# Kernel tuning notes

Hardware: AMD Instinct MI355X
Metric: run time of the kernel (lower is better)

Reference implementation:

```python
import jax, jax.numpy as jnp
import numpy as np
from jax import lax

DT_REF = 1.0
EPS = 1e-5


def layer_norm(x, g, b):
    m = jnp.mean(x, axis=-1, keepdims=True)
    v = jnp.mean(jnp.square(x - m), axis=-1, keepdims=True)
    return (x - m) * lax.rsqrt(v + EPS) * g + b


def pscan(A, X):
    # linear recurrence y_t = a_t*y_{t-1} + x_t along axis=1 (time)
    def comb(c1, c2):
        a1, x1 = c1
        a2, x2 = c2
        return a1 * a2, a2 * x1 + x2
    return lax.associative_scan(comb, (A, X), axis=1)[1]


def _forward(x_re, x_im, h_re, h_im, dt, flux_re, flux_im,
             ns_g, ns_b, conv_w, conv_b, E_re, E_im, F_re, F_im,
             mix_w, mix_b, nu, theta, src_w, src_b, gate_w, gate_b,
             lam_a, lam_b, nt_g, nt_b, r_w, r_b, e_w1, e_b1, e_w2, e_b2):
    B, T, D, H, W = x_re.shape
    x = lax.complex(x_re, x_im)                       # [B,T,D,H,W] complex

    # ---- spatial process: LN -> Clifford(3x3) conv -> complex residual ----
    xf = x.reshape(B * T, D, H, W)
    xr = jnp.concatenate([xf.real, xf.imag], axis=1)  # [BT,2D,H,W]
    xn = layer_norm(xr.transpose(0, 2, 3, 1), ns_g, ns_b).transpose(0, 3, 1, 2)
    xs = lax.conv_general_dilated(xn, conv_w, (1, 1), 'SAME',
                                  dimension_numbers=('NCHW', 'OIHW', 'NCHW'))
    xs = xs + conv_b[None, :, None, None]
    x = (xf + lax.complex(xs[:, :D], xs[:, D:])).reshape(B, T, D, H, W)

    # ---- eigenbasis encode ----
    Ec = lax.complex(E_re, E_im)                      # [D,D] complex basis
    xp = x.transpose(0, 1, 3, 4, 2)                   # [B,T,H,W,D]
    x_eigen = jnp.einsum('bthwd,de->bthwe', xp, Ec)
    x_mean = jnp.mean(x_eigen, axis=(2, 3))           # [B,T,D]

    # ---- flux tracker scan ----
    decay = jnp.exp(lax.complex(-jax.nn.softplus(nu), theta))  # [D]
    fcat = jnp.concatenate([x_mean.real, x_mean.imag], axis=-1) @ mix_w + mix_b
    x_mixed = lax.complex(fcat[..., :D], fcat[..., D:])        # [B,T,D]
    A_flux = jnp.broadcast_to(decay, (B, T, D))
    flux_seq = pscan(A_flux, x_mixed)                          # [B,T,D]
    decay_cum = jnp.cumprod(A_flux, axis=1)
    flux_seq = flux_seq + lax.complex(flux_re, flux_im)[:, None, :] * decay_cum

    ocat = jnp.concatenate([flux_seq.real, flux_seq.imag], axis=-1)  # [B,T,2D]
    s = ocat @ src_w + src_b
    source = lax.complex(s[..., :D], s[..., D:])                     # [B,T,D]
    gate = jax.nn.sigmoid(ocat @ gate_w + gate_b)                    # [B,T,D] real
    g = gate[:, :, None, None, :]
    forcing = x_eigen * g + source[:, :, None, None, :] * (1.0 - g)  # [B,T,H,W,D]

    # ---- transition operators (ZOH) ----
    dt_exp = jnp.broadcast_to(dt[None, :], (B, T))
    lam = lax.complex(-jax.nn.softplus(lam_a), lam_b)                # [D]
    op_decay = jnp.exp(lam[None, None, :] * (DT_REF * dt_exp)[:, :, None])  # [B,T,D]
    op_forcing = (op_decay - 1.0) / lam[None, None, :]

    u_t = forcing * op_forcing[:, :, None, None, :]
    h_prev = lax.complex(h_re, h_im).reshape(B, H, W, D)
    u_t = u_t.at[:, 0].add(h_prev * op_decay[:, 0][:, None, None, :])

    # ---- per-pixel/per-channel state scan over time ----
    A_state = jnp.broadcast_to(op_decay[:, :, None, None, :], u_t.shape)
    u_out = pscan(A_state, u_t)                       # [B,T,H,W,D]

    # ---- decode + temporal LN + MoE FFN ----
    Fc = lax.complex(F_re, F_im)
    x_dec = jnp.einsum('bthwd,de->bthwe', u_out, Fc)  # [B,T,H,W,D]
    of = x_dec.transpose(0, 1, 4, 2, 3).reshape(B * T, D, H, W)
    oc = jnp.concatenate([of.real, of.imag], axis=1).transpose(0, 2, 3, 1)  # [BT,H,W,2D]
    on = layer_norm(oc, nt_g, nt_b)
    xc = lax.complex(on[..., :D], on[..., D:])        # [BT,H,W,D]

    probs = jax.nn.softmax(on @ r_w + r_b, axis=-1)   # [BT,H,W,E]
    hid = jax.nn.gelu(jnp.einsum('nhwc,ecm->nhwem', on, e_w1) + e_b1)
    eo = jnp.einsum('nhwem,emc->nhwec', hid, e_w2) + e_b2
    moe = jnp.einsum('nhwec,nhwe->nhwc', eo, probs)   # [BT,H,W,2D]
    delta = lax.complex(moe[..., :D], moe[..., D:])

    x_outc = (xc + delta).transpose(0, 3, 1, 2).reshape(B, T, D, H, W)
    z = x + x_outc
    return jnp.concatenate([z.real, z.imag], axis=2)  # [B,T,2D,H,W] real


def setup_inputs() -> dict:
    B, T, D, H, W = 2, 16, 64, 64, 64
    C = 2 * D            # real channel width
    E, M = 4, 2 * C      # num_experts, ffn hidden = expand*2D, expand=2
    key = jax.random.key(0)
    ks = jax.random.split(key, 24)
    r = lambda k, shp, s=0.05: jax.random.normal(k, shp, jnp.float32) * s
    return dict(
        x_re=r(ks[0], (B, T, D, H, W), 0.5), x_im=r(ks[1], (B, T, D, H, W), 0.5),
        h_re=r(ks[2], (B * H * W, 1, D), 0.1), h_im=r(ks[3], (B * H * W, 1, D), 0.1),
        dt=jax.random.uniform(ks[4], (T,), jnp.float32, 0.5, 1.5),
        flux_re=r(ks[5], (B, D), 0.1), flux_im=r(ks[6], (B, D), 0.1),
        ns_g=jnp.ones((C,), jnp.float32), ns_b=jnp.zeros((C,), jnp.float32),
        conv_w=r(ks[7], (C, C, 3, 3)), conv_b=jnp.zeros((C,), jnp.float32),
        E_re=r(ks[8], (D, D), 0.1), E_im=r(ks[9], (D, D), 0.1),
        F_re=r(ks[10], (D, D), 0.1), F_im=r(ks[11], (D, D), 0.1),
        mix_w=r(ks[12], (C, C)), mix_b=jnp.zeros((C,), jnp.float32),
        nu=r(ks[13], (D,), 0.5) + 1.0, theta=r(ks[14], (D,), 0.5),
        src_w=r(ks[15], (C, C)), src_b=jnp.zeros((C,), jnp.float32),
        gate_w=r(ks[16], (C, D)), gate_b=jnp.zeros((D,), jnp.float32),
        lam_a=r(ks[17], (D,), 0.5) + 1.0, lam_b=r(ks[18], (D,), 0.5),
        nt_g=jnp.ones((C,), jnp.float32), nt_b=jnp.zeros((C,), jnp.float32),
        r_w=r(ks[19], (C, E)), r_b=jnp.zeros((E,), jnp.float32),
        e_w1=r(ks[20], (E, C, M)), e_b1=jnp.zeros((E, M), jnp.float32),
        e_w2=r(ks[21], (E, M, C)), e_b2=jnp.zeros((E, C), jnp.float32))


def reference(x_re, x_im, h_re, h_im, dt, flux_re, flux_im,
              ns_g, ns_b, conv_w, conv_b, E_re, E_im, F_re, F_im,
              mix_w, mix_b, nu, theta, src_w, src_b, gate_w, gate_b,
              lam_a, lam_b, nt_g, nt_b, r_w, r_b, e_w1, e_b1, e_w2, e_b2):
    return _forward(x_re, x_im, h_re, h_im, dt, flux_re, flux_im,
                    ns_g, ns_b, conv_w, conv_b, E_re, E_im, F_re, F_im,
                    mix_w, mix_b, nu, theta, src_w, src_b, gate_w, gate_b,
                    lam_a, lam_b, nt_g, nt_b, r_w, r_b, e_w1, e_b1, e_w2, e_b2)
```

## Files before the change

kernel.cpp:

```cpp
#include <hip/hip_runtime.h>


#define DEV static __device__ __forceinline__

typedef __attribute__((ext_vector_type(8))) short bf16x8;
typedef __attribute__((ext_vector_type(4))) float f32x4;
typedef __attribute__((ext_vector_type(16))) float f32x16;
typedef __attribute__((ext_vector_type(4))) unsigned int u32x4;

namespace {
constexpr int TN = 32;

DEV float sp_f(float x) { return x > 20.f ? x : log1pf(expf(x)); }
DEV unsigned short f2bf(float f) {
  unsigned int u = __float_as_uint(f);
  unsigned int r = (u + 0x7FFFu + ((u >> 16) & 1u)) >> 16;
  return (unsigned short)r;
}
DEV float bf2f(unsigned short s) { return __uint_as_float(((unsigned int)s) << 16); }
DEV unsigned int cvtpk(float lo, float hi) {
  unsigned int u;
  asm("v_cvt_pk_bf16_f32 %0, %1, %2" : "=v"(u) : "v"(lo), "v"(hi));
  return u;
}
DEV void split2(float a, float b, unsigned int& hi, unsigned int& lo) {
  unsigned short ha = f2bf(a), hb = f2bf(b);
  hi = (unsigned int)ha | ((unsigned int)hb << 16);
  float la = a - bf2f(ha), lb = b - bf2f(hb);
  lo = (unsigned int)f2bf(la) | ((unsigned int)f2bf(lb) << 16);
}
DEV float exp2_asm(float x) {
  float r;
  asm("v_exp_f32 %0, %1" : "=v"(r) : "v"(x));
  return r;
}
DEV float gelu_f(float x) {
  float e = exp2_asm(-2.4554863f * x);
  return x * __builtin_amdgcn_rcpf(1.f + e);
}
}

__global__ void k_repc(const float* __restrict__ cw, unsigned short* __restrict__ wcv) {
  int i = blockIdx.x * 256 + threadIdx.x;
  if (i >= 9 * 4 * 8 * 64 * 8) return;
  int j = i & 7, l = (i >> 3) & 63, ct = (i >> 9) & 7, cb = (i >> 12) & 3, k = i >> 14;
  int co = ct * 16 + (l & 15);
  int ci = cb * 32 + (l >> 4) * 8 + j;
  wcv[i] = f2bf(cw[((size_t)co * 128 + ci) * 9 + k]);
}

__global__ void k_repw(const float* __restrict__ w1, const float* __restrict__ w2,
                       const float* __restrict__ rw,
                       unsigned short* __restrict__ w1tp, unsigned short* __restrict__ w2p32,
                       unsigned short* __restrict__ rwp) {
  int i = blockIdx.x * 256 + threadIdx.x;
  if (i >= 262144 + 2048) return;
  if (i >= 262144) {
    int idx = i - 262144;
    int j = idx & 7, l = (idx >> 3) & 63, kt = idx >> 9;
    int col = l & 15;
    rwp[idx] = col < 4 ? f2bf(rw[(kt * 32 + (l >> 4) * 8 + j) * 4 + col]) : (unsigned short)0;
    return;
  }
  int half = i >> 17;
  int idx = i & 131071;
  int j = idx & 7, l = (idx >> 3) & 63;
  if (half == 0) {
    int kt = (idx >> 9) & 7, mtG = (idx >> 12) & 7, e = idx >> 15;
    int c = kt * 16 + (l >> 5) * 8 + j, m = mtG * 32 + (l & 31);
    w1tp[idx] = f2bf(w1[((size_t)e * 128 + c) * 256 + m]);
  } else {
    int ct = (idx >> 9) & 3, ktG = (idx >> 11) & 15, e = idx >> 15;
    int m = ktG * 16 + (l >> 5) * 8 + j, c = ct * 32 + (l & 31);
    w2p32[idx] = f2bf(w2[((size_t)e * 256 + m) * 128 + c]);
  }
}

__global__ void k_repEF(const float* __restrict__ Ere, const float* __restrict__ Eim,
                        const float* __restrict__ Fre, const float* __restrict__ Fim,
                        unsigned short* __restrict__ efb) {
  int i = blockIdx.x * 256 + threadIdx.x;
  if (i >= 32768) return;
  int sel = i >> 14;
  int f = i & 16383;
  float val;
  if (f < 8192) {
    int j = f & 7, l = (f >> 3) & 63, kt = (f >> 9) & 1, es = (f >> 10) & 1;
    int v = (f >> 11) & 1, eh = f >> 12;
    int d = kt * 32 + (l >> 4) * 8 + j;
    int e = eh * 32 + es * 16 + (l & 15);
    val = (v ? Eim : Ere)[d * 64 + e];
  } else {
    int g = f - 8192;
    int j = g & 7, l = (g >> 3) & 63, ds = (g >> 9) & 3;
    int v = (g >> 11) & 1, eh = g >> 12;
    int e = eh * 32 + (l >> 4) * 8 + j;
    int d = ds * 16 + (l & 15);
    val = (v ? Fim : Fre)[e * 64 + d];
  }
  unsigned short hv = f2bf(val);
  efb[i] = sel ? f2bf(val - bf2f(hv)) : hv;
}

__global__ __launch_bounds__(256) void k_ln_in(
    const float* __restrict__ xre, const float* __restrict__ xim,
    const float* __restrict__ gg, const float* __restrict__ bb,
    unsigned short* __restrict__ xnb, unsigned short* __restrict__ xfb) {
  int n = blockIdx.x >> 6, h = blockIdx.x & 63;
  __shared__ float xl[64][129];
  __shared__ float ps[4][64], ps2[4][64];
  __shared__ float mu[64], rs[64];
  int tid = threadIdx.x;
  int w = tid & 63, q = tid >> 6;
  size_t base = ((size_t)n * 4096 + h) * 64 + w;
  for (int d = q; d < 64; d += 4) {
    size_t o = base + (size_t)d * 4096;
    xl[w][d] = xre[o];
    xl[w][64 + d] = xim[o];
  }
  __syncthreads();
  float s = 0.f, s2 = 0.f;
  for (int c = q * 32; c < q * 32 + 32; ++c) { float v = xl[w][c]; s += v; s2 += v * v; }
  ps[q][w] = s; ps2[q][w] = s2;
  __syncthreads();
  if (tid < 64) {
    float a = 0.f, b2 = 0.f;
#pragma unroll
    for (int i = 0; i < 4; ++i) { a += ps[i][tid]; b2 += ps2[i][tid]; }
    float m = a * (1.f / 128.f);
    mu[tid] = m;
    rs[tid] = rsqrtf(b2 * (1.f / 128.f) - m * m + 1e-5f);
  }
  __syncthreads();
  size_t obase = ((size_t)n * 4096 + (size_t)h * 64) * 128;
  for (int idx = tid; idx < 64 * 64; idx += 256) {
    int q2 = idx >> 6, c2 = (idx & 63) * 2;
    float r0 = xl[q2][c2], r1 = xl[q2][c2 + 1];
    float v0 = (r0 - mu[q2]) * rs[q2] * gg[c2] + bb[c2];
    float v1 = (r1 - mu[q2]) * rs[q2] * gg[c2 + 1] + bb[c2 + 1];
    *(unsigned int*)&xnb[obase + (size_t)q2 * 128 + c2] = cvtpk(v0, v1);
    *(unsigned int*)&xfb[obase + (size_t)q2 * 128 + c2] = cvtpk(r0, r1);
  }
}

__global__ __launch_bounds__(256) void k_conv(
    const unsigned short* __restrict__ xnb, const unsigned short* __restrict__ wcv,
    const float* __restrict__ cbias, const unsigned short* __restrict__ xfb,
    unsigned short* __restrict__ XSf, unsigned short* __restrict__ XSl) {
  int n = blockIdx.x >> 6, h = blockIdx.x & 63;
  __shared__ __align__(16) short in_t[3 * 66 * 128];
  __shared__ float tr[64][66];
  int tid = threadIdx.x;
  int l = tid & 63;
  int w = __builtin_amdgcn_readfirstlane(tid >> 6);

  for (int it = 0; it < 13; ++it) {
    int ch = tid + it * 256;
    if (ch < 3168) {
      int ri = ch >> 4, cb16 = ch & 15;
      int rr = ri >= 132 ? 2 : (ri >= 66 ? 1 : 0);
      int wp = ri - rr * 66 - 1;
      int hh = h + rr - 1;
      uint4 v = make_uint4(0, 0, 0, 0);
      if ((unsigned)hh < 64u && (unsigned)wp < 64u)
        v = *(const uint4*)(xnb + ((size_t)(n * 4096 + hh * 64 + wp) << 7) + cb16 * 8);
      int off = (ri * 256 + cb16 * 16) ^ ((ri & 7) << 4);
      *(uint4*)((char*)in_t + off) = v;
    }
  }
  __syncthreads();

  f32x4 acc[4][2];
#pragma unroll
  for (int pt = 0; pt < 4; ++pt) { acc[pt][0] = {0,0,0,0}; acc[pt][1] = {0,0,0,0}; }

#pragma unroll
  for (int kh = 0; kh < 3; ++kh) {
#pragma unroll
    for (int kw = 0; kw < 3; ++kw) {
      int k = kh * 3 + kw;
#pragma unroll
      for (int cb = 0; cb < 4; ++cb) {
        const unsigned short* wb = wcv + ((((size_t)(k * 4 + cb) * 8) + 2 * w) * 64 + l) * 8;
        bf16x8 b0 = *(const bf16x8*)wb;
        bf16x8 b1 = *(const bf16x8*)(wb + 64 * 8);
#pragma unroll
        for (int pt = 0; pt < 4; ++pt) {
          int ri = kh * 66 + pt * 16 + (l & 15) + kw;
          int off = (ri * 256 + cb * 64 + (l >> 4) * 16) ^ ((ri & 7) << 4);
          bf16x8 a = *(const bf16x8*)((const char*)in_t + off);
          acc[pt][0] = __builtin_amdgcn_mfma_f32_16x16x32_bf16(a, b0, acc[pt][0], 0, 0, 0);
          acc[pt][1] = __builtin_amdgcn_mfma_f32_16x16x32_bf16(a, b1, acc[pt][1], 0, 0, 0);
        }
      }
    }
  }

  for (int pass = 0; pass < 2; ++pass) {
    __syncthreads();
    if ((w >> 1) == pass) {
      int ctl = w & 1;
#pragma unroll
      for (int ct = 0; ct < 2; ++ct) {
        int col = ctl * 32 + ct * 16 + (l & 15);
        float bias = cbias[pass * 64 + col];
#pragma unroll
        for (int pt = 0; pt < 4; ++pt) {
          int pxb = pt * 16 + (l >> 4) * 4;
          size_t xfo = ((size_t)(n * 4096 + h * 64 + pxb)) * 128 + pass * 64 + col;
#pragma unroll
          for (int r = 0; r < 4; ++r)
            tr[col][pxb + r] = acc[pt][ct][r] + bias + bf2f(xfb[xfo + (size_t)r * 128]);
        }
      }
    }
    __syncthreads();
#pragma unroll
    for (int q = 0; q < 2; ++q) {
      int it = tid + q * 256;
      int ptl = it >> 7, kt = (it >> 6) & 1, lf = it & 63;
      int dbase = kt * 32 + (lf >> 4) * 8;
      int px = ptl * 16 + (lf & 15);
      unsigned int hw[4], lw[4];
#pragma unroll
      for (int u = 0; u < 4; ++u)
        split2(tr[dbase + 2 * u][px], tr[dbase + 2 * u + 1][px], hw[u], lw[u]);
      size_t base = ((((size_t)n * 256 + h * 4 + ptl) * 2 + pass) * 2 + kt) * 512 + lf * 8;
      *(uint4*)(XSf + base) = make_uint4(hw[0], hw[1], hw[2], hw[3]);
      *(uint4*)(XSl + base) = make_uint4(lw[0], lw[1], lw[2], lw[3]);
    }
    __syncthreads();
  }
}

__global__ __launch_bounds__(256) void k_xmean(const unsigned short* __restrict__ XSf,
                                               const unsigned short* __restrict__ XSl,
                                               float2* __restrict__ Xm) {
  int nd = blockIdx.x;
  int n = nd >> 6, d = nd & 63;
  int kt = d >> 5, hs = (d >> 3) & 3, j = d & 7;
  int tid = threadIdx.x;
  float sr = 0.f, si = 0.f;
  for (int p = tid; p < 4096; p += 256) {
    int ptg = p >> 4, c = p & 15;
    size_t b0 = ((((size_t)n * 256 + ptg) * 2 + 0) * 2 + kt) * 512 + (hs * 16 + c) * 8 + j;
    size_t b1 = ((((size_t)n * 256 + ptg) * 2 + 1) * 2 + kt) * 512 + (hs * 16 + c) * 8 + j;
    sr += bf2f(XSf[b0]) + bf2f(XSl[b0]);
    si += bf2f(XSf[b1]) + bf2f(XSl[b1]);
  }
  __shared__ float r1[256], r2[256];
  r1[tid] = sr; r2[tid] = si;
  __syncthreads();
  for (int s = 128; s > 0; s >>= 1) {
    if (tid < s) { r1[tid] += r1[tid + s]; r2[tid] += r2[tid + s]; }
    __syncthreads();
  }
  if (tid == 0) Xm[nd] = make_float2(r1[0] * (1.f / 4096.f), r2[0] * (1.f / 4096.f));
}

__global__ void k_chainA(const float2* __restrict__ Xm, const float* __restrict__ Ere,
                         const float* __restrict__ Eim, const float* __restrict__ mixw,
                         const float* __restrict__ mixb, float2* __restrict__ xmix) {
  int n = blockIdx.x;
  int tid = threadIdx.x;
  __shared__ float2 xm[64];
  __shared__ float cat[128];
  __shared__ float fc[128];
  if (tid < 64) xm[tid] = Xm[n * 64 + tid];
  __syncthreads();
  if (tid < 64) {
    float ar = 0.f, ai = 0.f;
    for (int d = 0; d < 64; ++d) {
      float2 x = xm[d];
      float er = Ere[d * 64 + tid], ei = Eim[d * 64 + tid];
      ar += x.x * er - x.y * ei;
      ai += x.x * ei + x.y * er;
    }
    cat[tid] = ar; cat[64 + tid] = ai;
  }
  __syncthreads();
  {
    float f = mixb[tid];
    for (int i = 0; i < 128; ++i) f += cat[i] * mixw[i * 128 + tid];
    fc[tid] = f;
  }
  __syncthreads();
  if (tid < 64) xmix[n * 64 + tid] = make_float2(fc[tid], fc[64 + tid]);
}

__global__ void k_chainB(const float2* __restrict__ xmix, const float* __restrict__ nu,
                         const float* __restrict__ th, const float* __restrict__ fre,
                         const float* __restrict__ fim, float2* __restrict__ fs) {
  int tid = threadIdx.x;
  int b = tid >> 6, d = tid & 63;
  float r = expf(-sp_f(nu[d]));
  float dr = r * cosf(th[d]), di = r * sinf(th[d]);
  float yr = 0.f, yi = 0.f, cr = 1.f, ci = 0.f;
  float fr = fre[b * 64 + d], fi = fim[b * 64 + d];
  for (int t = 0; t < 16; ++t) {
    int n = b * 16 + t;
    float ncr = cr * dr - ci * di, nci = cr * di + ci * dr;
    cr = ncr; ci = nci;
    float2 xm = xmix[n * 64 + d];
    float nyr = dr * yr - di * yi + xm.x;
    float nyi = dr * yi + di * yr + xm.y;
    yr = nyr; yi = nyi;
    fs[n * 64 + d] = make_float2(yr + fr * cr - fi * ci, yi + fr * ci + fi * cr);
  }
}

__global__ void k_chainC(const float2* __restrict__ fs, const float* __restrict__ srcw,
                         const float* __restrict__ srcb, const float* __restrict__ gw,
                         const float* __restrict__ gbv, const float* __restrict__ la,
                         const float* __restrict__ lbv, const float* __restrict__ dt,
                         float* __restrict__ abo) {
  int n = blockIdx.x;
  int t = n & 15;
  int tid = threadIdx.x;
  __shared__ float oc[128];
  __shared__ float sl[128];
  if (tid < 64) { float2 v = fs[n * 64 + tid]; oc[tid] = v.x; oc[64 + tid] = v.y; }
  __syncthreads();
  {
    float s = srcb[tid];
    for (int i = 0; i < 128; ++i) s += oc[i] * srcw[i * 128 + tid];
    sl[tid] = s;
  }
  __syncthreads();
  if (tid < 64) {
    float gv = gbv[tid];
    for (int i = 0; i < 128; ++i) gv += oc[i] * gw[i * 64 + tid];
    float g = 1.f / (1.f + expf(-gv));
    float lr = -sp_f(la[tid]), li = lbv[tid];
    float dtv = dt[t];
    float er = expf(lr * dtv);
    float odr = er * cosf(li * dtv), odi = er * sinf(li * dtv);
    float inv = 1.f / (lr * lr + li * li);
    float nx = odr - 1.f, ny = odi;
    float ofr = (nx * lr + ny * li) * inv, ofi = (ny * lr - nx * li) * inv;
    float s1r = sl[tid] * (1.f - g), s1i = sl[64 + tid] * (1.f - g);
    float* ap = abo + ((size_t)n * 64 + tid) * 8;
    ap[0] = g * ofr;
    ap[1] = g * ofi;
    ap[2] = s1r * ofr - s1i * ofi;
    ap[3] = s1r * ofi + s1i * ofr;
    ap[4] = odr;
    ap[5] = odi;
    ap[6] = 0.f; ap[7] = 0.f;
  }
}

__global__ __launch_bounds__(128) void k_state(
    const unsigned short* __restrict__ XSf, const unsigned short* __restrict__ XSl,
    const unsigned short* __restrict__ efb,
    const float* __restrict__ abo, const float* __restrict__ hre,
    const float* __restrict__ him, const float* __restrict__ ntg,
    const float* __restrict__ ntb, unsigned short* __restrict__ onb) {
  int bq = blockIdx.x;
  int b = bq >> 8, pt = bq & 255;
  int p0 = pt * 16;
  int tid = threadIdx.x;
  int l = tid & 63;
  int eh = __builtin_amdgcn_readfirstlane(tid >> 6);
  int c = l & 15, h4 = l >> 4;

  __shared__ float xpart[2 * 64 * 17];
  __shared__ float ntgl[128], ntbl[128];
  ntgl[tid] = ntg[tid]; ntbl[tid] = ntb[tid];

  const unsigned short* Ehi = efb;
  const unsigned short* Fhi = efb + 8192;
  const unsigned short* Elo = efb + 16384;
  const unsigned short* Flo = efb + 24576;

  bf16x8 erh[2][2], eihh[2][2], erl[2][2], eil[2][2];
#pragma unroll
  for (int es = 0; es < 2; ++es)
#pragma unroll
    for (int kt = 0; kt < 2; ++kt) {
      size_t o = (size_t)(eh * 4096 + es * 1024 + kt * 512 + l * 8);
      erh[es][kt] = *(const bf16x8*)(Ehi + o);
      eihh[es][kt] = *(const bf16x8*)(Ehi + o + 2048);
      erl[es][kt] = *(const bf16x8*)(Elo + o);
      eil[es][kt] = *(const bf16x8*)(Elo + o + 2048);
    }
  bf16x8 frh[4], fih[4], frl[4], fil[4];
#pragma unroll
  for (int ds = 0; ds < 4; ++ds) {
    size_t o = (size_t)(eh * 4096 + ds * 512 + l * 8);
    frh[ds] = *(const bf16x8*)(Fhi + o);
    fih[ds] = *(const bf16x8*)(Fhi + o + 2048);
    frl[ds] = *(const bf16x8*)(Flo + o);
    fil[ds] = *(const bf16x8*)(Flo + o + 2048);
  }

  float yre[2][4], yim[2][4];
#pragma unroll
  for (int es = 0; es < 2; ++es)
#pragma unroll
    for (int r = 0; r < 4; ++r) { yre[es][r] = 0.f; yim[es][r] = 0.f; }

  __syncthreads();

  const f32x4 Z = {0.f, 0.f, 0.f, 0.f};
  for (int t = 0; t < 16; ++t) {
    int n = b * 16 + t;
    bf16x8 xh0[2], xh1[2], xq0[2], xq1[2];
#pragma unroll
    for (int kt = 0; kt < 2; ++kt) {
      size_t b0 = ((((size_t)n * 256 + pt) * 2 + 0) * 2 + kt) * 512 + l * 8;
      size_t b1 = ((((size_t)n * 256 + pt) * 2 + 1) * 2 + kt) * 512 + l * 8;
      xh0[kt] = *(const bf16x8*)(XSf + b0);
      xh1[kt] = *(const bf16x8*)(XSf + b1);
      xq0[kt] = *(const bf16x8*)(XSl + b0);
      xq1[kt] = *(const bf16x8*)(XSl + b1);
    }
#pragma unroll
    for (int es = 0; es < 2; ++es) {
      f32x4 a1 = Z, a2 = Z, a3 = Z, a4 = Z;
#pragma unroll
      for (int kt = 0; kt < 2; ++kt) {
        a1 = __builtin_amdgcn_mfma_f32_16x16x32_bf16(erh[es][kt], xh0[kt], a1, 0, 0, 0);
        a1 = __builtin_amdgcn_mfma_f32_16x16x32_bf16(erh[es][kt], xq0[kt], a1, 0, 0, 0);
        a1 = __builtin_amdgcn_mfma_f32_16x16x32_bf16(erl[es][kt], xh0[kt], a1, 0, 0, 0);
        a2 = __builtin_amdgcn_mfma_f32_16x16x32_bf16(eihh[es][kt], xh1[kt], a2, 0, 0, 0);
        a2 = __builtin_amdgcn_mfma_f32_16x16x32_bf16(eihh[es][kt], xq1[kt], a2, 0, 0, 0);
        a2 = __builtin_amdgcn_mfma_f32_16x16x32_bf16(eil[es][kt], xh1[kt], a2, 0, 0, 0);
        a3 = __builtin_amdgcn_mfma_f32_16x16x32_bf16(eihh[es][kt], xh0[kt], a3, 0, 0, 0);
        a3 = __builtin_amdgcn_mfma_f32_16x16x32_bf16(eihh[es][kt], xq0[kt], a3, 0, 0, 0);
        a3 = __builtin_amdgcn_mfma_f32_16x16x32_bf16(eil[es][kt], xh0[kt], a3, 0, 0, 0);
        a4 = __builtin_amdgcn_mfma_f32_16x16x32_bf16(erh[es][kt], xh1[kt], a4, 0, 0, 0);
        a4 = __builtin_amdgcn_mfma_f32_16x16x32_bf16(erh[es][kt], xq1[kt], a4, 0, 0, 0);
        a4 = __builtin_amdgcn_mfma_f32_16x16x32_bf16(erl[es][kt], xh1[kt], a4, 0, 0, 0);
      }
#pragma unroll
      for (int r = 0; r < 4; ++r) {
        int e = eh * 32 + es * 16 + 4 * h4 + r;
        const float* ap = abo + ((size_t)n * 64 + e) * 8;
        float4 cv = *(const float4*)ap;
        float2 ov = *(const float2*)(ap + 4);
        float xr_ = a1[r] - a2[r], xi_ = a3[r] + a4[r];
        float ur = xr_ * cv.x - xi_ * cv.y + cv.z;
        float ui = xr_ * cv.y + xi_ * cv.x + cv.w;
        if (t == 0) {
          size_t ho = ((size_t)(b * 4096 + p0 + c)) * 64 + e;
          float hr = hre[ho], hi = him[ho];
          ur += hr * ov.x - hi * ov.y;
          ui += hr * ov.y + hi * ov.x;
        }
        float nyr = ov.x * yre[es][r] - ov.y * yim[es][r] + ur;
        float nyi = ov.x * yim[es][r] + ov.y * yre[es][r] + ui;
        yre[es][r] = nyr; yim[es][r] = nyi;
      }
    }
    unsigned int hr_[2][2], lr_[2][2], hi_[2][2], li_[2][2];
#pragma unroll
    for (int es = 0; es < 2; ++es) {
      split2(yre[es][0], yre[es][1], hr_[es][0], lr_[es][0]);
      split2(yre[es][2], yre[es][3], hr_[es][1], lr_[es][1]);
      split2(yim[es][0], yim[es][1], hi_[es][0], li_[es][0]);
      split2(yim[es][2], yim[es][3], hi_[es][1], li_[es][1]);
    }
    int base_src = c + 16 * (2 * (h4 & 1));
    int hsel = h4 >> 1;
    u32x4 urh, uih, url, uil;
#pragma unroll
    for (int jj = 0; jj < 4; ++jj) {
      int src = base_src + 16 * (jj >> 1);
      unsigned int t0, t1;
      t0 = (unsigned int)__shfl((int)hr_[0][jj & 1], src);
      t1 = (unsigned int)__shfl((int)hr_[1][jj & 1], src);
      urh[jj] = hsel ? t1 : t0;
      t0 = (unsigned int)__shfl((int)hi_[0][jj & 1], src);
      t1 = (unsigned int)__shfl((int)hi_[1][jj & 1], src);
      uih[jj] = hsel ? t1 : t0;
      t0 = (unsigned int)__shfl((int)lr_[0][jj & 1], src);
      t1 = (unsigned int)__shfl((int)lr_[1][jj & 1], src);
      url[jj] = hsel ? t1 : t0;
      t0 = (unsigned int)__shfl((int)li_[0][jj & 1], src);
      t1 = (unsigned int)__shfl((int)li_[1][jj & 1], src);
      uil[jj] = hsel ? t1 : t0;
    }
    bf16x8 ybrh = __builtin_bit_cast(bf16x8, urh);
    bf16x8 ybih = __builtin_bit_cast(bf16x8, uih);
    bf16x8 ybrl = __builtin_bit_cast(bf16x8, url);
    bf16x8 ybil = __builtin_bit_cast(bf16x8, uil);
    float v[2][4][4];
#pragma unroll
    for (int ds = 0; ds < 4; ++ds) {
      f32x4 d1 = Z, d2 = Z, d3 = Z, d4 = Z;
      d1 = __builtin_amdgcn_mfma_f32_16x16x32_bf16(frh[ds], ybrh, d1, 0, 0, 0);
      d1 = __builtin_amdgcn_mfma_f32_16x16x32_bf16(frh[ds], ybrl, d1, 0, 0, 0);
      d1 = __builtin_amdgcn_mfma_f32_16x16x32_bf16(frl[ds], ybrh, d1, 0, 0, 0);
      d2 = __builtin_amdgcn_mfma_f32_16x16x32_bf16(fih[ds], ybih, d2, 0, 0, 0);
      d2 = __builtin_amdgcn_mfma_f32_16x16x32_bf16(fih[ds], ybil, d2, 0, 0, 0);
      d2 = __builtin_amdgcn_mfma_f32_16x16x32_bf16(fil[ds], ybih, d2, 0, 0, 0);
      d3 = __builtin_amdgcn_mfma_f32_16x16x32_bf16(fih[ds], ybrh, d3, 0, 0, 0);
      d3 = __builtin_amdgcn_mfma_f32_16x16x32_bf16(fih[ds], ybrl, d3, 0, 0, 0);
      d3 = __builtin_amdgcn_mfma_f32_16x16x32_bf16(fil[ds], ybrh, d3, 0, 0, 0);
      d4 = __builtin_amdgcn_mfma_f32_16x16x32_bf16(frh[ds], ybih, d4, 0, 0, 0);
      d4 = __builtin_amdgcn_mfma_f32_16x16x32_bf16(frh[ds], ybil, d4, 0, 0, 0);
      d4 = __builtin_amdgcn_mfma_f32_16x16x32_bf16(frl[ds], ybih, d4, 0, 0, 0);
#pragma unroll
      for (int r = 0; r < 4; ++r) {
        v[0][ds][r] = d1[r] - d2[r];
        v[1][ds][r] = d3[r] + d4[r];
      }
    }
    bool own = (eh == (t & 1));
    if (!own) {
#pragma unroll
      for (int p = 0; p < 2; ++p)
#pragma unroll
        for (int ds = 0; ds < 4; ++ds)
#pragma unroll
          for (int r = 0; r < 4; ++r)
            xpart[(p * 64 + ds * 16 + 4 * h4 + r) * 17 + c] = v[p][ds][r];
    }
    __syncthreads();
    if (own) {
      float s = 0.f, s2 = 0.f;
#pragma unroll
      for (int p = 0; p < 2; ++p)
#pragma unroll
        for (int ds = 0; ds < 4; ++ds)
#pragma unroll
          for (int r = 0; r < 4; ++r) {
            float q2 = v[p][ds][r] + xpart[(p * 64 + ds * 16 + 4 * h4 + r) * 17 + c];
            v[p][ds][r] = q2;
            s += q2; s2 += q2 * q2;
          }
      s += __shfl_xor(s, 16); s += __shfl_xor(s, 32);
      s2 += __shfl_xor(s2, 16); s2 += __shfl_xor(s2, 32);
      float mu = s * (1.f / 128.f);
      float rsv = rsqrtf(s2 * (1.f / 128.f) - mu * mu + 1e-5f);
      size_t ob = ((size_t)(n * 4096 + p0 + c)) * 128;
#pragma unroll
      for (int p = 0; p < 2; ++p)
#pragma unroll
        for (int ds = 0; ds < 4; ++ds) {
          int ch = p * 64 + ds * 16 + 4 * h4;
          float l0 = (v[p][ds][0] - mu) * rsv * ntgl[ch + 0] + ntbl[ch + 0];
          float l1 = (v[p][ds][1] - mu) * rsv * ntgl[ch + 1] + ntbl[ch + 1];
          float l2 = (v[p][ds][2] - mu) * rsv * ntgl[ch + 2] + ntbl[ch + 2];
          float l3 = (v[p][ds][3] - mu) * rsv * ntgl[ch + 3] + ntbl[ch + 3];
          *(unsigned int*)&onb[ob + ch] = cvtpk(l0, l1);
          *(unsigned int*)&onb[ob + ch + 2] = cvtpk(l2, l3);
        }
    }
    __syncthreads();
  }
}

__global__ __launch_bounds__(256) void k_moe2(
    const unsigned short* __restrict__ onb, const unsigned short* __restrict__ w1tp,
    const unsigned short* __restrict__ w2p32, const unsigned short* __restrict__ rwp,
    const float* __restrict__ rb, const float* __restrict__ b1, const float* __restrict__ b2,
    const unsigned short* __restrict__ XSf, const unsigned short* __restrict__ XSl,
    float* __restrict__ out) {
  int n = blockIdx.x >> 6, ptile = blockIdx.x & 63;
  int p0 = ptile * 64;
  __shared__ __align__(16) short At[64 * 128];
  __shared__ __align__(16) float buf[4160];
  __shared__ float pr[64][4];
  int tid = threadIdx.x;
  int l = tid & 63;
  int w = __builtin_amdgcn_readfirstlane(tid >> 6);
  int h = l >> 5, s = l & 31;
  float* b1l = buf;
  float* b2l = buf + 1024;

  for (int i = tid; i < 1024; i += 256) b1l[i] = b1[i];
  for (int i = tid; i < 512; i += 256) b2l[i] = b2[i];

  {
    const char* gsrc = (const char*)onb + ((size_t)n * 4096 + p0) * 256;
#pragma unroll
    for (int it = 0; it < 4; ++it) {
      int ch = tid + it * 256;
      int row = ch >> 4, cb = (ch & 15) * 16;
      float4 v = *(const float4*)(gsrc + (size_t)row * 256 + cb);
      int off = (row * 256 + cb) ^ ((row & 7) << 4);
      *(float4*)((char*)At + off) = v;
    }
  }
  __syncthreads();

  {
    f32x4 acc = {0.f, 0.f, 0.f, 0.f};
#pragma unroll
    for (int kt = 0; kt < 4; ++kt) {
      int row = w * 16 + (l & 15);
      int off = (row * 256 + kt * 64 + (l >> 4) * 16) ^ ((row & 7) << 4);
      bf16x8 aa = *(const bf16x8*)((const char*)At + off);
      bf16x8 bb = *(const bf16x8*)(rwp + ((size_t)kt * 64 + l) * 8);
      acc = __builtin_amdgcn_mfma_f32_16x16x32_bf16(aa, bb, acc, 0, 0, 0);
    }
    int e = l & 15;
    float rbv = e < 4 ? rb[e] : 0.f;
#pragma unroll
    for (int r = 0; r < 4; ++r) {
      float lg = acc[r] + rbv;
      float m = fmaxf(lg, __shfl_xor(lg, 1));
      m = fmaxf(m, __shfl_xor(m, 2));
      float ex = __expf(lg - m);
      float sm = ex + __shfl_xor(ex, 1);
      sm += __shfl_xor(sm, 2);
      float p = ex * __builtin_amdgcn_rcpf(sm);
      if (e < 4) pr[w * 16 + (l >> 4) * 4 + r][e] = p;
    }
  }
  __syncthreads();

  int pw = w & 1, mh = w >> 1;
  int rowb = pw * 32 + s;
  int swz = (rowb & 7) << 4;

  float macc[4][16];
#pragma unroll
  for (int ct = 0; ct < 4; ++ct)
#pragma unroll
    for (int r = 0; r < 16; ++r) macc[ct][r] = 0.f;

  const f32x16 Z16 = {0.f, 0.f, 0.f, 0.f, 0.f, 0.f, 0.f, 0.f,
                      0.f, 0.f, 0.f, 0.f, 0.f, 0.f, 0.f, 0.f};

  for (int e = 0; e < 4; ++e) {
    u32x4 af[8];
#pragma unroll
    for (int mt = 0; mt < 4; ++mt) {
      f32x16 acc = Z16;
#pragma unroll
      for (int kt = 0; kt < 8; ++kt) {
        bf16x8 a = *(const bf16x8*)(
            w1tp + ((((size_t)e * 8 + (mh * 4 + mt)) * 8 + kt) * 64 + l) * 8);
        int off = (rowb * 256 + kt * 32 + h * 16) ^ swz;
        bf16x8 b = *(const bf16x8*)((const char*)At + off);
        acc = __builtin_amdgcn_mfma_f32_32x32x16_bf16(a, b, acc, 0, 0, 0);
      }
      unsigned int hpk[8];
#pragma unroll
      for (int i2 = 0; i2 < 8; ++i2) {
        int r0 = 2 * i2;
        int m0 = mh * 128 + mt * 32 + (r0 & 3) + 8 * (r0 >> 2) + 4 * h;
        float2 bv = *(const float2*)&b1l[e * 256 + m0];
        hpk[i2] = cvtpk(gelu_f(acc[r0] + bv.x), gelu_f(acc[r0 + 1] + bv.y));
      }
#pragma unroll
      for (int hf = 0; hf < 2; ++hf) {
        unsigned int pA = hpk[4 * hf + 0], pB = hpk[4 * hf + 1];
        unsigned int pC = hpk[4 * hf + 2], pD = hpk[4 * hf + 3];
        unsigned int Z0 = h ? pC : pA, Z1 = h ? pD : pB;
        unsigned int S0 = h ? pA : pC, S1 = h ? pB : pD;
        unsigned int Ss0 = (unsigned int)__shfl_xor((int)S0, 32);
        unsigned int Ss1 = (unsigned int)__shfl_xor((int)S1, 32);
        u32x4 fr2;
        fr2.x = h ? Ss0 : Z0;
        fr2.y = h ? Ss1 : Z1;
        fr2.z = h ? Z0 : Ss0;
        fr2.w = h ? Z1 : Ss1;
        af[mt * 2 + hf] = fr2;
      }
    }
    float prv[16];
#pragma unroll
    for (int r = 0; r < 16; ++r) {
      int px = pw * 32 + (r & 3) + 8 * (r >> 2) + 4 * h;
      prv[r] = pr[px][e];
    }
#pragma unroll
    for (int ct = 0; ct < 4; ++ct) {
      f32x16 acc = Z16;
#pragma unroll
      for (int kt = 0; kt < 8; ++kt) {
        bf16x8 bf = *(const bf16x8*)(
            w2p32 + ((((size_t)e * 16 + (mh * 8 + kt)) * 4 + ct) * 64 + l) * 8);
        bf16x8 a = __builtin_bit_cast(bf16x8, af[kt]);
        acc = __builtin_amdgcn_mfma_f32_32x32x16_bf16(a, bf, acc, 0, 0, 0);
      }
      float b2v = mh ? 0.f : b2l[e * 128 + ct * 32 + s];
#pragma unroll
      for (int r = 0; r < 16; ++r) macc[ct][r] += (acc[r] + b2v) * prv[r];
    }
  }

#pragma unroll
  for (int ph = 0; ph < 2; ++ph) {
    int ct0 = ph * 2;
    __syncthreads();
    if (mh == 1) {
#pragma unroll
      for (int g = 0; g < 8; ++g) {
        int ct = ct0 + (g >> 2), q = (g & 3) * 4;
        float4 v = make_float4(macc[ct][q], macc[ct][q + 1], macc[ct][q + 2], macc[ct][q + 3]);
        *(float4*)&buf[((g * 2 + pw) * 64 + l) * 4] = v;
      }
    }
    __syncthreads();
    if (mh == 0) {
#pragma unroll
      for (int g = 0; g < 8; ++g) {
        float4 v = *(const float4*)&buf[((g * 2 + pw) * 64 + l) * 4];
        int ct = ct0 + (g >> 2), q = (g & 3) * 4;
        macc[ct][q] += v.x; macc[ct][q + 1] += v.y;
        macc[ct][q + 2] += v.z; macc[ct][q + 3] += v.w;
      }
    }
    __syncthreads();
    if (mh == 0) {
#pragma unroll
      for (int cti = 0; cti < 2; ++cti) {
        int ct = ct0 + cti;
        int cc = ct * 32 + s;
        int cl = cc - ph * 64;
#pragma unroll
        for (int r = 0; r < 16; ++r) {
          int px = pw * 32 + (r & 3) + 8 * (r >> 2) + 4 * h;
          int aoff = (px * 256 + cc * 2) ^ ((px & 7) << 4);
          float onv = bf2f(((unsigned short*)At)[aoff >> 1]);
          buf[px * 65 + cl] = macc[ct][r] + onv;
        }
      }
    }
    __syncthreads();
    for (int idx = tid; idx < 64 * 64; idx += 256) {
      int px = idx & 63, cl = idx >> 6;
      int p = p0 + px;
      size_t el = ((((size_t)n * 256 + (p >> 4)) * 2 + ph) * 2 + (cl >> 5)) * 512
                + (((cl >> 3) & 3) * 16 + (p & 15)) * 8 + (cl & 7);
      float resid = bf2f(XSf[el]) + bf2f(XSl[el]);
      out[((size_t)n * 128 + ph * 64 + cl) * 4096 + p0 + px] = resid + buf[px * 65 + cl];
    }
  }
}

extern "C" void kernel_launch(void* const* d_in, const int* in_sizes, int n_in,
                              void* d_out, int out_size, void* d_ws, size_t ws_size,
                              hipStream_t stream) {
  const float* xre = (const float*)d_in[0];
  const float* xim = (const float*)d_in[1];
  const float* hre = (const float*)d_in[2];
  const float* him = (const float*)d_in[3];
  const float* dt = (const float*)d_in[4];
  const float* fre = (const float*)d_in[5];
  const float* fim = (const float*)d_in[6];
  const float* nsg = (const float*)d_in[7];
  const float* nsb = (const float*)d_in[8];
  const float* cw = (const float*)d_in[9];
  const float* cb = (const float*)d_in[10];
  const float* Ere = (const float*)d_in[11];
  const float* Eim = (const float*)d_in[12];
  const float* Fre = (const float*)d_in[13];
  const float* Fim = (const float*)d_in[14];
  const float* mixw = (const float*)d_in[15];
  const float* mixb = (const float*)d_in[16];
  const float* nu = (const float*)d_in[17];
  const float* th = (const float*)d_in[18];
  const float* srcw = (const float*)d_in[19];
  const float* srcb = (const float*)d_in[20];
  const float* gw = (const float*)d_in[21];
  const float* gbv = (const float*)d_in[22];
  const float* la = (const float*)d_in[23];
  const float* lb = (const float*)d_in[24];
  const float* ntg = (const float*)d_in[25];
  const float* ntb = (const float*)d_in[26];
  const float* rw = (const float*)d_in[27];
  const float* rb = (const float*)d_in[28];
  const float* w1 = (const float*)d_in[29];
  const float* b1 = (const float*)d_in[30];
  const float* w2 = (const float*)d_in[31];
  const float* b2 = (const float*)d_in[32];

  unsigned short* XSf = (unsigned short*)d_ws;
  unsigned short* XSl = XSf + 16777216;
  unsigned short* onb16 = XSl + 16777216;
  unsigned short* wcv = onb16 + 16777216;
  unsigned short* w1tp = wcv + 147456;
  unsigned short* w2p32 = w1tp + 131072;
  unsigned short* rwp = w2p32 + 131072;
  unsigned short* efb = rwp + 2048;
  float* smf = (float*)(efb + 32768);
  float* abo = smf;
  float2* Xm = (float2*)(abo + 16384);
  float2* xmix = Xm + TN * 64;
  float2* fsb = xmix + TN * 64;

  float* out = (float*)d_out;
  unsigned short* xnb = (unsigned short*)d_out;
  unsigned short* xfb = xnb + 16777216;

  hipLaunchKernelGGL(k_repc, dim3(576), dim3(256), 0, stream, cw, wcv);
  hipLaunchKernelGGL(k_repw, dim3(1033), dim3(256), 0, stream, w1, w2, rw, w1tp, w2p32, rwp);
  hipLaunchKernelGGL(k_repEF, dim3(128), dim3(256), 0, stream, Ere, Eim, Fre, Fim, efb);
  hipLaunchKernelGGL(k_ln_in, dim3(TN * 64), dim3(256), 0, stream, xre, xim, nsg, nsb, xnb, xfb);
  hipLaunchKernelGGL(k_conv, dim3(TN * 64), dim3(256), 0, stream, xnb, wcv, cb, xfb, XSf, XSl);
  hipLaunchKernelGGL(k_xmean, dim3(TN * 64), dim3(256), 0, stream, XSf, XSl, Xm);
  hipLaunchKernelGGL(k_chainA, dim3(TN), dim3(128), 0, stream, Xm, Ere, Eim, mixw, mixb, xmix);
  hipLaunchKernelGGL(k_chainB, dim3(1), dim3(128), 0, stream, xmix, nu, th, fre, fim, fsb);
  hipLaunchKernelGGL(k_chainC, dim3(TN), dim3(128), 0, stream, fsb, srcw, srcb, gw, gbv, la, lb,
                     dt, abo);
  hipLaunchKernelGGL(k_state, dim3(512), dim3(128), 0, stream, XSf, XSl, efb, abo, hre, him,
                     ntg, ntb, onb16);
  hipLaunchKernelGGL(k_moe2, dim3(TN * 64), dim3(256), 0, stream, onb16, w1tp, w2p32, rwp, rb,
                     b1, b2, XSf, XSl, out);
  (void)in_sizes; (void)n_in; (void)out_size; (void)ws_size;
}
```

Before: 500.0 us.

## Fold MoE gate probability into hidden activations and accumulate experts in MFMA

The router probability now scales the GELU hidden activations (per token row) before the second GEMM, so all experts accumulate directly into one set of MFMA accumulators instead of per-expert temporaries that were scaled and added by hand. The second GEMM is interleaved into the first's loop, so the af fragment array no longer has to stay live. The b2 bias weighted by the probabilities is added once in the epilogue from a new shared array. This cuts VALU multiply-adds and register pressure, at the cost of rounding the probability-scaled activations to bf16.

```diff
diff --git a/kernel.cpp b/kernel.cpp
--- a/kernel.cpp
+++ b/kernel.cpp
@@ -563,15 +563,15 @@
   __shared__ __align__(16) short At[64 * 128];
   __shared__ __align__(16) float buf[4160];
   __shared__ float pr[64][4];
+  __shared__ float b2ls[512];
   int tid = threadIdx.x;
   int l = tid & 63;
   int w = __builtin_amdgcn_readfirstlane(tid >> 6);
   int h = l >> 5, s = l & 31;
   float* b1l = buf;
-  float* b2l = buf + 1024;
 
   for (int i = tid; i < 1024; i += 256) b1l[i] = b1[i];
-  for (int i = tid; i < 512; i += 256) b2l[i] = b2[i];
+  for (int i = tid; i < 512; i += 256) b2ls[i] = b2[i];
 
   {
     const char* gsrc = (const char*)onb + ((size_t)n * 4096 + p0) * 256;
@@ -616,17 +616,14 @@
   int rowb = pw * 32 + s;
   int swz = (rowb & 7) << 4;
 
-  float macc[4][16];
-#pragma unroll
-  for (int ct = 0; ct < 4; ++ct)
-#pragma unroll
-    for (int r = 0; r < 16; ++r) macc[ct][r] = 0.f;
-
   const f32x16 Z16 = {0.f, 0.f, 0.f, 0.f, 0.f, 0.f, 0.f, 0.f,
                       0.f, 0.f, 0.f, 0.f, 0.f, 0.f, 0.f, 0.f};
+  f32x16 macc4[4];
+#pragma unroll
+  for (int ct = 0; ct < 4; ++ct) macc4[ct] = Z16;
 
   for (int e = 0; e < 4; ++e) {
-    u32x4 af[8];
+    float pe = pr[rowb][e];
 #pragma unroll
     for (int mt = 0; mt < 4; ++mt) {
       f32x16 acc = Z16;
@@ -644,7 +641,7 @@
         int r0 = 2 * i2;
         int m0 = mh * 128 + mt * 32 + (r0 & 3) + 8 * (r0 >> 2) + 4 * h;
         float2 bv = *(const float2*)&b1l[e * 256 + m0];
-        hpk[i2] = cvtpk(gelu_f(acc[r0] + bv.x), gelu_f(acc[r0 + 1] + bv.y));
+        hpk[i2] = cvtpk(gelu_f(acc[r0] + bv.x) * pe, gelu_f(acc[r0 + 1] + bv.y) * pe);
       }
 #pragma unroll
       for (int hf = 0; hf < 2; ++hf) {
@@ -659,28 +656,15 @@
         fr2.y = h ? Ss1 : Z1;
         fr2.z = h ? Z0 : Ss0;
         fr2.w = h ? Z1 : Ss1;
-        af[mt * 2 + hf] = fr2;
-      }
-    }
-    float prv[16];
-#pragma unroll
-    for (int r = 0; r < 16; ++r) {
-      int px = pw * 32 + (r & 3) + 8 * (r >> 2) + 4 * h;
-      prv[r] = pr[px][e];
-    }
-#pragma unroll
-    for (int ct = 0; ct < 4; ++ct) {
-      f32x16 acc = Z16;
-#pragma unroll
-      for (int kt = 0; kt < 8; ++kt) {
-        bf16x8 bf = *(const bf16x8*)(
-            w2p32 + ((((size_t)e * 16 + (mh * 8 + kt)) * 4 + ct) * 64 + l) * 8);
-        bf16x8 a = __builtin_bit_cast(bf16x8, af[kt]);
-        acc = __builtin_amdgcn_mfma_f32_32x32x16_bf16(a, bf, acc, 0, 0, 0);
-      }
-      float b2v = mh ? 0.f : b2l[e * 128 + ct * 32 + s];
-#pragma unroll
-      for (int r = 0; r < 16; ++r) macc[ct][r] += (acc[r] + b2v) * prv[r];
+        bf16x8 a2 = __builtin_bit_cast(bf16x8, fr2);
+        int ktg = mt * 2 + hf;
+#pragma unroll
+        for (int ct = 0; ct < 4; ++ct) {
+          bf16x8 bf = *(const bf16x8*)(
+              w2p32 + ((((size_t)e * 16 + (mh * 8 + ktg)) * 4 + ct) * 64 + l) * 8);
+          macc4[ct] = __builtin_amdgcn_mfma_f32_32x32x16_bf16(a2, bf, macc4[ct], 0, 0, 0);
+        }
+      }
     }
   }
 
@@ -692,7 +676,8 @@
 #pragma unroll
       for (int g = 0; g < 8; ++g) {
         int ct = ct0 + (g >> 2), q = (g & 3) * 4;
-        float4 v = make_float4(macc[ct][q], macc[ct][q + 1], macc[ct][q + 2], macc[ct][q + 3]);
+        float4 v = make_float4(macc4[ct][q], macc4[ct][q + 1], macc4[ct][q + 2],
+                               macc4[ct][q + 3]);
         *(float4*)&buf[((g * 2 + pw) * 64 + l) * 4] = v;
       }
     }
@@ -702,8 +687,8 @@
       for (int g = 0; g < 8; ++g) {
         float4 v = *(const float4*)&buf[((g * 2 + pw) * 64 + l) * 4];
         int ct = ct0 + (g >> 2), q = (g & 3) * 4;
-        macc[ct][q] += v.x; macc[ct][q + 1] += v.y;
-        macc[ct][q + 2] += v.z; macc[ct][q + 3] += v.w;
+        macc4[ct][q] += v.x; macc4[ct][q + 1] += v.y;
+        macc4[ct][q + 2] += v.z; macc4[ct][q + 3] += v.w;
       }
     }
     __syncthreads();
@@ -718,7 +703,9 @@
           int px = pw * 32 + (r & 3) + 8 * (r >> 2) + 4 * h;
           int aoff = (px * 256 + cc * 2) ^ ((px & 7) << 4);
           float onv = bf2f(((unsigned short*)At)[aoff >> 1]);
-          buf[px * 65 + cl] = macc[ct][r] + onv;
+          float bsum = pr[px][0] * b2ls[cc] + pr[px][1] * b2ls[128 + cc] +
+                       pr[px][2] * b2ls[256 + cc] + pr[px][3] * b2ls[384 + cc];
+          buf[px * 65 + cl] = macc4[ct][r] + bsum + onv;
         }
       }
     }
```

Result: slower. 667.1 us (+33.4%).
